# Kernel tuning notes

Hardware: AMD Instinct MI355X
Metric: run time of the kernel (lower is better)

The kernel has to match this reference:

```python
import jax, jax.numpy as jnp
import numpy as np

N_HEAD = 32
N_KV_HEAD = 8
ROPE_THETA = 500000.0


def rotate_half(x):
    d = x.shape[-1] // 2
    return jnp.concatenate((-x[..., d:], x[..., :d]), axis=-1)


def setup_inputs() -> dict:
    key = jax.random.key(0)
    ks = jax.random.split(key, 5)
    C = 2048
    B, T = 2, 2048
    s = 1.0 / np.sqrt(C)
    return {
        "x": jax.random.normal(ks[0], (B, T, C), dtype=jnp.float32),
        "Wq": jax.random.normal(ks[1], (C, C), dtype=jnp.float32) * s,
        "Wk": jax.random.normal(ks[2], (C, 512), dtype=jnp.float32) * s,
        "Wv": jax.random.normal(ks[3], (C, 512), dtype=jnp.float32) * s,
        "Wo": jax.random.normal(ks[4], (C, C), dtype=jnp.float32) * s,
    }


def reference(x, Wq, Wk, Wv, Wo):
    B, T, C = x.shape
    H, KV = N_HEAD, N_KV_HEAD
    D = C // H
    n_rep = H // KV

    q = (x @ Wq).reshape(B, T, H, D).transpose(0, 2, 1, 3)   # [B,H,T,D]
    k = (x @ Wk).reshape(B, T, KV, D).transpose(0, 2, 1, 3)  # [B,KV,T,D]
    v = (x @ Wv).reshape(B, T, KV, D).transpose(0, 2, 1, 3)  # [B,KV,T,D]

    # RoPE: cos/sin of shape [1,1,T,D], broadcast over batch and heads
    inv_freq = 1.0 / (ROPE_THETA ** (jnp.arange(0, D, 2, dtype=jnp.float32) / D))
    freqs = jnp.arange(T, dtype=jnp.float32)[:, None] * inv_freq[None, :]  # [T,D/2]
    emb = jnp.concatenate((freqs, freqs), axis=-1)  # [T,D]
    cos = jnp.cos(emb)[None, None].astype(x.dtype)
    sin = jnp.sin(emb)[None, None].astype(x.dtype)

    q = q * cos + rotate_half(q) * sin
    k = k * cos + rotate_half(k) * sin

    # repeat_kv (GQA expansion): [B,KV,T,D] -> [B,H,T,D]
    k = jnp.repeat(k, n_rep, axis=1)
    v = jnp.repeat(v, n_rep, axis=1)

    scale = 1.0 / jnp.sqrt(jnp.asarray(D, dtype=x.dtype))
    scores = jnp.einsum("bhqd,bhkd->bhqk", q, k) * scale  # [B,H,T,T]
    causal = jnp.tril(jnp.ones((T, T), dtype=bool))
    scores = jnp.where(causal[None, None], scores, jnp.finfo(scores.dtype).min)
    attn = jax.nn.softmax(scores, axis=-1)
    y = jnp.einsum("bhqk,bhkd->bhqd", attn, v)  # [B,H,T,D]
    y = y.transpose(0, 2, 1, 3).reshape(B, T, C)
    return y @ Wo
```

## Files before the change

### kernel.cpp

```cpp
#include <hip/hip_runtime.h>

using u16 = unsigned short;
using u32 = unsigned int;

typedef __attribute__((ext_vector_type(8))) __bf16 bf16x8;
typedef __attribute__((ext_vector_type(4))) float f32x4;
typedef __attribute__((ext_vector_type(16))) float f32x16;

#define DEVI __device__ __forceinline__

DEVI float bf2f(u16 u) {
  union { u32 i; float f; } v; v.i = ((u32)u) << 16; return v.f;
}
DEVI u16 f2bf(float f) {
  union { float f; u32 u; } v; v.f = f;
  u32 u = v.u;
  u32 r = (u + 0x7fffu + ((u >> 16) & 1u)) >> 16;
  return (u16)r;
}
DEVI u32 pkbf(float a, float b) {
  union { __bf16 h[2]; u32 u; } t;
  t.h[0] = (__bf16)a; t.h[1] = (__bf16)b;
  return t.u;
}

DEVI void gload16(const u16* g, u16* l) {
  __builtin_amdgcn_global_load_lds(
      (const __attribute__((address_space(1))) void*)g,
      (__attribute__((address_space(3))) void*)l, 16, 0, 0);
}

__global__ __launch_bounds__(256) void cvt_bf16_f32(const float* __restrict__ in,
                                                    u16* __restrict__ out, int n8) {
  int i = blockIdx.x * 256 + threadIdx.x;
  if (i >= n8) return;
  const float4* fin = (const float4*)in;
  float4 a = fin[i * 2], b = fin[i * 2 + 1];
  u16 o[8] = {f2bf(a.x), f2bf(a.y), f2bf(a.z), f2bf(a.w),
              f2bf(b.x), f2bf(b.y), f2bf(b.z), f2bf(b.w)};
  ((uint4*)out)[i] = *(const uint4*)o;
}

DEVI void tcvt64_body(const float* in, u16* out, int R, int Cc, int c0, int r0, int t,
                      u16 (*tile)[72]) {
  {
    int row = t >> 2, part = t & 3;
    const float* src = in + (size_t)(r0 + row) * Cc + c0 + part * 16;
    float4 f0 = ((const float4*)src)[0];
    float4 f1 = ((const float4*)src)[1];
    float4 f2 = ((const float4*)src)[2];
    float4 f3 = ((const float4*)src)[3];
    u16 v[16] = {f2bf(f0.x), f2bf(f0.y), f2bf(f0.z), f2bf(f0.w),
                 f2bf(f1.x), f2bf(f1.y), f2bf(f1.z), f2bf(f1.w),
                 f2bf(f2.x), f2bf(f2.y), f2bf(f2.z), f2bf(f2.w),
                 f2bf(f3.x), f2bf(f3.y), f2bf(f3.z), f2bf(f3.w)};
    *(uint4*)&tile[row][part * 16]     = ((const uint4*)v)[0];
    *(uint4*)&tile[row][part * 16 + 8] = ((const uint4*)v)[1];
  }
  __syncthreads();
  {
    int c = t & 63, rq = t >> 6;
    u16 v[16];
#pragma unroll
    for (int i = 0; i < 16; i++) v[i] = tile[rq * 16 + i][c];
    u16* dst = out + (size_t)(c0 + c) * R + r0 + rq * 16;
    ((uint4*)dst)[0] = ((const uint4*)v)[0];
    ((uint4*)dst)[1] = ((const uint4*)v)[1];
  }
}

__global__ __launch_bounds__(256) void transpose_cvt64(const float* __restrict__ in,
                                                       u16* __restrict__ out,
                                                       int R, int Cc) {
  __shared__ u16 tile[64][72];
  tcvt64_body(in, out, R, Cc, blockIdx.x * 64, blockIdx.y * 64, threadIdx.x, tile);
}

__global__ __launch_bounds__(256) void transpose_wqkv(const float* __restrict__ Wq,
                                                      const float* __restrict__ Wk,
                                                      const float* __restrict__ Wv,
                                                      u16* __restrict__ out) {
  __shared__ u16 tile[64][72];
  int bx = blockIdx.x;
  const float* in;
  u16* dst;
  int Cc, c0;
  if (bx < 32)      { in = Wq; dst = out;                        Cc = 2048; c0 = bx * 64; }
  else if (bx < 40) { in = Wk; dst = out + (size_t)2048 * 2048;  Cc = 512;  c0 = (bx - 32) * 64; }
  else              { in = Wv; dst = out + (size_t)2560 * 2048;  Cc = 512;  c0 = (bx - 40) * 64; }
  tcvt64_body(in, dst, 2048, Cc, c0, blockIdx.y * 64, threadIdx.x, tile);
}

__global__ __launch_bounds__(256) void transpose_sl64(const u16* __restrict__ in, int ldin,
                                                      u16* __restrict__ out,
                                                      int R, int Cc) {
  __shared__ u16 tile[64][72];
  int c0 = blockIdx.x * 64, r0 = blockIdx.y * 64;
  int t = threadIdx.x;
  {
    int row = t >> 2, part = t & 3;
    const u16* src = in + (size_t)(r0 + row) * ldin + c0 + part * 16;
    uint4 a = ((const uint4*)src)[0];
    uint4 b = ((const uint4*)src)[1];
    *(uint4*)&tile[row][part * 16]     = a;
    *(uint4*)&tile[row][part * 16 + 8] = b;
  }
  __syncthreads();
  {
    int c = t & 63, rq = t >> 6;
    u16 v[16];
#pragma unroll
    for (int i = 0; i < 16; i++) v[i] = tile[rq * 16 + i][c];
    u16* dst = out + (size_t)(c0 + c) * R + r0 + rq * 16;
    ((uint4*)dst)[0] = ((const uint4*)v)[0];
    ((uint4*)dst)[1] = ((const uint4*)v)[1];
  }
}

DEVI void cstore(u16* C, size_t idx, float v)   { C[idx] = f2bf(v); }
DEVI void cstore(float* C, size_t idx, float v) { C[idx] = v; }

template <typename TO, bool ROPE>
__global__ __launch_bounds__(256) void gemm128(const u16* __restrict__ A,
                                               const u16* __restrict__ Bt,
                                               TO* __restrict__ C,
                                               int M, int N, int K) {
  __shared__ u16 As[2 * 128 * 32];
  __shared__ u16 Bs[2 * 128 * 32];
  int tid = threadIdx.x, wid = tid >> 6, lane = tid & 63;
  int quad = lane >> 4, l15 = lane & 15;

  int nwg = gridDim.x * gridDim.y;
  int bid = blockIdx.y * gridDim.x + blockIdx.x;
  int swz = (bid & 7) * (nwg >> 3) + (bid >> 3);
  int bx = swz % gridDim.x, by = swz / gridDim.x;
  int m0 = by * 128, n0 = bx * 128;
  int wm = (wid >> 1) * 64, wn = (wid & 1) * 64;

  int r0s = wid * 16 + (lane >> 2);
  int r1s = 64 + wid * 16 + (lane >> 2);
  int cblk = lane & 3;
  int cs0 = (cblk ^ ((r0s >> 1) & 3)) * 8;
  int cs1 = (cblk ^ ((r1s >> 1) & 3)) * 8;
  u16* lA0 = As + wid * 512 + lane * 8;
  u16* lA1 = As + (4 + wid) * 512 + lane * 8;
  u16* lB0 = Bs + wid * 512 + lane * 8;
  u16* lB1 = Bs + (4 + wid) * 512 + lane * 8;
  const u16* gA0 = A + (size_t)(m0 + r0s) * K + cs0;
  const u16* gA1 = A + (size_t)(m0 + r1s) * K + cs1;
  const u16* gB0 = Bt + (size_t)(n0 + r0s) * K + cs0;
  const u16* gB1 = Bt + (size_t)(n0 + r1s) * K + cs1;

  f32x4 acc[4][4];
  for (int i = 0; i < 4; i++)
    for (int j = 0; j < 4; j++) acc[i][j] = f32x4{0.f, 0.f, 0.f, 0.f};

  gload16(gA0, lA0);
  gload16(gA1, lA1);
  gload16(gB0, lB0);
  gload16(gB1, lB1);
  __builtin_amdgcn_s_waitcnt(0x0F70);
  __syncthreads();

  int cur = 0;
  for (int k0 = 0; k0 < K; k0 += 32) {
    int nb = cur ^ 1;
    if (k0 + 32 < K) {
      gload16(gA0 + k0 + 32, lA0 + nb * 4096);
      gload16(gA1 + k0 + 32, lA1 + nb * 4096);
      gload16(gB0 + k0 + 32, lB0 + nb * 4096);
      gload16(gB1 + k0 + 32, lB1 + nb * 4096);
    }
    const u16* Ab = As + cur * 4096;
    const u16* Bb = Bs + cur * 4096;
    bf16x8 af[4], bf_[4];
    for (int mi = 0; mi < 4; mi++) {
      int row = wm + mi * 16 + l15;
      af[mi] = *(const bf16x8*)(Ab + row * 32 + ((quad ^ ((row >> 1) & 3)) * 8));
    }
    for (int ni = 0; ni < 4; ni++) {
      int row = wn + ni * 16 + l15;
      bf_[ni] = *(const bf16x8*)(Bb + row * 32 + ((quad ^ ((row >> 1) & 3)) * 8));
    }
    for (int mi = 0; mi < 4; mi++)
      for (int ni = 0; ni < 4; ni++)
        acc[mi][ni] = __builtin_amdgcn_mfma_f32_16x16x32_bf16(af[mi], bf_[ni], acc[mi][ni], 0, 0, 0);
    __builtin_amdgcn_s_waitcnt(0x0F70);
    __syncthreads();
    cur = nb;
  }

  if (ROPE) {
#pragma unroll
    for (int ni = 0; ni < 2; ni++) {
      int nc = n0 + wn + ni * 16;
      if (nc < 2560) {
        float scale = (nc < 2048) ? 0.18033688f : 1.0f;
        float inv = exp2f(-(float)(ni * 16 + l15) * 0.59161152f);
#pragma unroll
        for (int mi = 0; mi < 4; mi++)
#pragma unroll
          for (int r = 0; r < 4; r++) {
            int t = (m0 + wm + mi * 16 + quad * 4 + r) & 2047;
            float sn, cs;
            __sincosf((float)t * inv, &sn, &cs);
            float xl = acc[mi][ni][r], xh = acc[mi][ni + 2][r];
            acc[mi][ni][r]     = (xl * cs - xh * sn) * scale;
            acc[mi][ni + 2][r] = (xh * cs + xl * sn) * scale;
          }
      }
    }
  }

  for (int mi = 0; mi < 4; mi++)
    for (int ni = 0; ni < 4; ni++)
      for (int r = 0; r < 4; r++) {
        int row = m0 + wm + mi * 16 + quad * 4 + r;
        int col = n0 + wn + ni * 16 + l15;
        cstore(C, (size_t)row * N + col, acc[mi][ni][r]);
      }
}

__global__ __launch_bounds__(256) void attn64(const u16* __restrict__ QKV,
                                              const u16* __restrict__ Vt,
                                              u16* __restrict__ Y) {
  __shared__ u16 Ks[2 * 64 * 64];
  __shared__ u16 Vst[2 * 64 * 64];

  int tid = threadIdx.x, wid = tid >> 6, lane = tid & 63;
  int l31 = lane & 31, hi = lane >> 5;
  int bh = blockIdx.y, b = bh >> 5, h = bh & 31, kvh = h >> 2;
  int p = blockIdx.x;

  int kr  = wid * 8 + (lane >> 3);
  int kgn = lane & 7;
  const u16* gK0 = QKV + (size_t)(b * 2048 + kr) * 3072 + 2048 + kvh * 64
                 + ((kgn ^ (kr & 7)) * 8);
  u16* lK0 = Ks + wid * 512 + lane * 8;

  int vr = tid >> 3, vg = tid & 7;
  const u16* gV0 = Vt + (size_t)(kvh * 64 + vr) * 4096 + b * 2048 + vg * 8;
  u16* lV0 = Vst + vr * 64 + ((vg ^ (vr & 7)) * 8);

  for (int pass = 0; pass < 2; pass++) {
    int j   = pass ? (15 - p) : p;
    int q0w = j * 128 + wid * 32;
    int qg  = q0w + l31;

    bf16x8 qf[4];
    {
      const u16* qp = QKV + (size_t)(b * 2048 + qg) * 3072 + h * 64 + hi * 8;
#pragma unroll
      for (int dh = 0; dh < 4; dh++) qf[dh] = *(const bf16x8*)(qp + dh * 16);
    }

    f32x16 o0, o1;
#pragma unroll
    for (int i = 0; i < 16; i++) { o0[i] = 0.f; o1[i] = 0.f; }
    float zsum = 0.f;

    int nkt = 2 * (j + 1);

    {
      uint4 va = *(const uint4*)(gV0);
      uint4 vb = *(const uint4*)(gV0 + 32 * 4096);
      gload16(gK0, lK0);
      gload16(gK0 + 32 * 3072, lK0 + 2048);
      __builtin_amdgcn_s_waitcnt(0x0F70);
      *(uint4*)(lV0)        = va;
      *(uint4*)(lV0 + 2048) = vb;
    }
    __syncthreads();

    int cur = 0;
    for (int kt = 0; kt < nkt; kt++) {
      int kbase = kt * 64;
      int nxt = cur ^ 1;
      bool more = (kt + 1 < nkt);
      uint4 va, vb;
      if (more) {
        size_t ko = (size_t)(kbase + 64);
        va = *(const uint4*)(gV0 + ko);
        vb = *(const uint4*)(gV0 + 32 * 4096 + ko);
        gload16(gK0 + ko * 3072, lK0 + nxt * 4096);
        gload16(gK0 + ko * 3072 + 32 * 3072, lK0 + nxt * 4096 + 2048);
      }

      const u16* Kb = Ks + cur * 4096;
      const u16* Vb = Vst + cur * 4096;
#pragma unroll
      for (int sub = 0; sub < 2; sub++) {
        int kb = kbase + sub * 32;
        if (kb > q0w) break;

        f32x16 s;
#pragma unroll
        for (int i = 0; i < 16; i++) s[i] = 0.f;
#pragma unroll
        for (int dh = 0; dh < 4; dh++) {
          int g = (dh * 2 + hi) ^ (l31 & 7);
          bf16x8 kf = *(const bf16x8*)(Kb + (sub * 32 + l31) * 64 + g * 8);
          s = __builtin_amdgcn_mfma_f32_32x32x16_bf16(kf, qf[dh], s, 0, 0, 0);
        }

        float pb[16];
        if (kb < q0w) {
#pragma unroll
          for (int r = 0; r < 16; r++) {
            float pv = exp2f(s[r]);
            zsum += pv;
            pb[r] = pv;
          }
        } else {
#pragma unroll
          for (int r = 0; r < 16; r++) {
            int key = kb + (r & 3) + 8 * (r >> 2) + 4 * hi;
            float pv = (key <= qg) ? exp2f(s[r]) : 0.f;
            zsum += pv;
            pb[r] = pv;
          }
        }

#pragma unroll
        for (int kk = 0; kk < 2; kk++) {
          const float* pp = pb + kk * 8;
          u32 a01 = pkbf(pp[0], pp[1]);
          u32 a23 = pkbf(pp[2], pp[3]);
          u32 a45 = pkbf(pp[4], pp[5]);
          u32 a67 = pkbf(pp[6], pp[7]);
          asm volatile("v_permlane32_swap_b32 %0, %1" : "+v"(a01), "+v"(a45));
          asm volatile("v_permlane32_swap_b32 %0, %1" : "+v"(a23), "+v"(a67));
          union { u32 w[4]; bf16x8 v; } pf;
          pf.w[0] = a01; pf.w[1] = a23; pf.w[2] = a45; pf.w[3] = a67;
          int kgr = sub * 4 + kk * 2 + hi;
          const u16* vp = Vb + l31 * 64 + ((kgr ^ (l31 & 7)) * 8);
          bf16x8 v0 = *(const bf16x8*)(vp);
          bf16x8 v1 = *(const bf16x8*)(vp + 2048);
          o0 = __builtin_amdgcn_mfma_f32_32x32x16_bf16(pf.v, v0, o0, 0, 0, 0);
          o1 = __builtin_amdgcn_mfma_f32_32x32x16_bf16(pf.v, v1, o1, 0, 0, 0);
        }
      }

      if (more) {
        __builtin_amdgcn_s_waitcnt(0x0F70);
        *(uint4*)(lV0 + nxt * 4096)        = va;
        *(uint4*)(lV0 + nxt * 4096 + 2048) = vb;
      }
      __syncthreads();
      cur = nxt;
    }

    float zf = zsum + __shfl_xor(zsum, 32);

#pragma unroll
    for (int r = 0; r < 16; r++) {
      int qr = (r & 3) + 8 * (r >> 2) + 4 * hi;
      float zr = __shfl(zf, qr, 64);
      float inv = 1.f / zr;
      size_t row = (size_t)(b * 2048 + q0w + qr);
      Y[row * 2048 + h * 64 + l31]      = f2bf(o0[r] * inv);
      Y[row * 2048 + h * 64 + 32 + l31] = f2bf(o1[r] * inv);
    }
  }
}

extern "C" void kernel_launch(void* const* d_in, const int* in_sizes, int n_in,
                              void* d_out, int out_size, void* d_ws, size_t ws_size,
                              hipStream_t stream) {
  const float* x  = (const float*)d_in[0];
  const float* Wq = (const float*)d_in[1];
  const float* Wk = (const float*)d_in[2];
  const float* Wv = (const float*)d_in[3];
  const float* Wo = (const float*)d_in[4];
  float* outp = (float*)d_out;

  u16* xb    = (u16*)d_ws;
  u16* WqkvT = xb + 8388608;
  u16* QKV   = WqkvT + 6291456;
  u16* Vt    = QKV + 12582912;
  u16* Yb    = xb;
  u16* WoT   = WqkvT;

  cvt_bf16_f32<<<4096, 256, 0, stream>>>(x, xb, 1048576);

  transpose_wqkv<<<dim3(48, 32), 256, 0, stream>>>(Wq, Wk, Wv, WqkvT);

  gemm128<u16, true><<<dim3(24, 32), 256, 0, stream>>>(xb, WqkvT, QKV, 4096, 3072, 2048);

  transpose_sl64<<<dim3(8, 64), 256, 0, stream>>>(QKV + 2560, 3072, Vt, 4096, 512);

  attn64<<<dim3(8, 64), 256, 0, stream>>>(QKV, Vt, Yb);

  transpose_cvt64<<<dim3(32, 32), 256, 0, stream>>>(Wo, WoT, 2048, 2048);
  gemm128<float, false><<<dim3(16, 32), 256, 0, stream>>>(Yb, WoT, outp, 4096, 2048, 2048);
}
```

Measured before the change: 310.5 us.

## Fuse both causal query passes into one K/V sweep sharing tiles

The attention kernel previously handled query blocks p and 15-p in two sequential passes, each streaming its own K/V tiles from global memory. Now both query tiles are processed together in a single sweep over the longer causal range, so K/V tiles are loaded once and reused for both sets of MFMAs. This halves K/V traffic and barrier count for the overlapping range, but doubles accumulator registers (four f32x16 outputs plus two Q fragments), which may lower occupancy or cause spills.

```diff
diff --git a/kernel.cpp b/kernel.cpp
--- a/kernel.cpp
+++ b/kernel.cpp
@@ -28,6 +28,18 @@
   __builtin_amdgcn_global_load_lds(
       (const __attribute__((address_space(1))) void*)g,
       (__attribute__((address_space(3))) void*)l, 16, 0, 0);
+}
+
+DEVI bf16x8 packP(const float* pp) {
+  u32 a01 = pkbf(pp[0], pp[1]);
+  u32 a23 = pkbf(pp[2], pp[3]);
+  u32 a45 = pkbf(pp[4], pp[5]);
+  u32 a67 = pkbf(pp[6], pp[7]);
+  asm volatile("v_permlane32_swap_b32 %0, %1" : "+v"(a01), "+v"(a45));
+  asm volatile("v_permlane32_swap_b32 %0, %1" : "+v"(a23), "+v"(a67));
+  union { u32 w[4]; bf16x8 v; } pf;
+  pf.w[0] = a01; pf.w[1] = a23; pf.w[2] = a45; pf.w[3] = a67;
+  return pf.v;
 }
 
 __global__ __launch_bounds__(256) void cvt_bf16_f32(const float* __restrict__ in,
@@ -231,6 +243,7 @@
   int l31 = lane & 31, hi = lane >> 5;
   int bh = blockIdx.y, b = bh >> 5, h = bh & 31, kvh = h >> 2;
   int p = blockIdx.x;
+  int jA = p, jB = 15 - p;
 
   int kr  = wid * 8 + (lane >> 3);
   int kgn = lane & 7;
@@ -242,124 +255,179 @@
   const u16* gV0 = Vt + (size_t)(kvh * 64 + vr) * 4096 + b * 2048 + vg * 8;
   u16* lV0 = Vst + vr * 64 + ((vg ^ (vr & 7)) * 8);
 
-  for (int pass = 0; pass < 2; pass++) {
-    int j   = pass ? (15 - p) : p;
-    int q0w = j * 128 + wid * 32;
-    int qg  = q0w + l31;
-
-    bf16x8 qf[4];
-    {
-      const u16* qp = QKV + (size_t)(b * 2048 + qg) * 3072 + h * 64 + hi * 8;
-#pragma unroll
-      for (int dh = 0; dh < 4; dh++) qf[dh] = *(const bf16x8*)(qp + dh * 16);
-    }
-
-    f32x16 o0, o1;
-#pragma unroll
-    for (int i = 0; i < 16; i++) { o0[i] = 0.f; o1[i] = 0.f; }
-    float zsum = 0.f;
-
-    int nkt = 2 * (j + 1);
-
-    {
-      uint4 va = *(const uint4*)(gV0);
-      uint4 vb = *(const uint4*)(gV0 + 32 * 4096);
-      gload16(gK0, lK0);
-      gload16(gK0 + 32 * 3072, lK0 + 2048);
-      __builtin_amdgcn_s_waitcnt(0x0F70);
-      *(uint4*)(lV0)        = va;
-      *(uint4*)(lV0 + 2048) = vb;
-    }
-    __syncthreads();
-
-    int cur = 0;
-    for (int kt = 0; kt < nkt; kt++) {
-      int kbase = kt * 64;
-      int nxt = cur ^ 1;
-      bool more = (kt + 1 < nkt);
-      uint4 va, vb;
-      if (more) {
-        size_t ko = (size_t)(kbase + 64);
-        va = *(const uint4*)(gV0 + ko);
-        vb = *(const uint4*)(gV0 + 32 * 4096 + ko);
-        gload16(gK0 + ko * 3072, lK0 + nxt * 4096);
-        gload16(gK0 + ko * 3072 + 32 * 3072, lK0 + nxt * 4096 + 2048);
-      }
-
-      const u16* Kb = Ks + cur * 4096;
-      const u16* Vb = Vst + cur * 4096;
-#pragma unroll
-      for (int sub = 0; sub < 2; sub++) {
-        int kb = kbase + sub * 32;
-        if (kb > q0w) break;
-
-        f32x16 s;
-#pragma unroll
-        for (int i = 0; i < 16; i++) s[i] = 0.f;
+  int q0wA = jA * 128 + wid * 32, qgA = q0wA + l31;
+  int q0wB = jB * 128 + wid * 32, qgB = q0wB + l31;
+
+  bf16x8 qfA[4], qfB[4];
+  {
+    const u16* qpA = QKV + (size_t)(b * 2048 + qgA) * 3072 + h * 64 + hi * 8;
+    const u16* qpB = QKV + (size_t)(b * 2048 + qgB) * 3072 + h * 64 + hi * 8;
+#pragma unroll
+    for (int dh = 0; dh < 4; dh++) {
+      qfA[dh] = *(const bf16x8*)(qpA + dh * 16);
+      qfB[dh] = *(const bf16x8*)(qpB + dh * 16);
+    }
+  }
+
+  f32x16 o0A, o1A, o0B, o1B;
+#pragma unroll
+  for (int i = 0; i < 16; i++) { o0A[i] = 0.f; o1A[i] = 0.f; o0B[i] = 0.f; o1B[i] = 0.f; }
+  float zsumA = 0.f, zsumB = 0.f;
+
+  int nkt = 2 * (jB + 1);
+
+  {
+    uint4 va = *(const uint4*)(gV0);
+    uint4 vb = *(const uint4*)(gV0 + 32 * 4096);
+    gload16(gK0, lK0);
+    gload16(gK0 + 32 * 3072, lK0 + 2048);
+    __builtin_amdgcn_s_waitcnt(0x0F70);
+    *(uint4*)(lV0)        = va;
+    *(uint4*)(lV0 + 2048) = vb;
+  }
+  __syncthreads();
+
+  int cur = 0;
+  for (int kt = 0; kt < nkt; kt++) {
+    int kbase = kt * 64;
+    int nxt = cur ^ 1;
+    bool more = (kt + 1 < nkt);
+    uint4 va, vb;
+    if (more) {
+      size_t ko = (size_t)(kbase + 64);
+      va = *(const uint4*)(gV0 + ko);
+      vb = *(const uint4*)(gV0 + 32 * 4096 + ko);
+      gload16(gK0 + ko * 3072, lK0 + nxt * 4096);
+      gload16(gK0 + ko * 3072 + 32 * 3072, lK0 + nxt * 4096 + 2048);
+    }
+
+    const u16* Kb = Ks + cur * 4096;
+    const u16* Vb = Vst + cur * 4096;
+#pragma unroll
+    for (int sub = 0; sub < 2; sub++) {
+      int kb = kbase + sub * 32;
+      if (kb > q0wB) break;
+      if (kb <= q0wA) {
+        f32x16 sA, sB;
+#pragma unroll
+        for (int i = 0; i < 16; i++) { sA[i] = 0.f; sB[i] = 0.f; }
 #pragma unroll
         for (int dh = 0; dh < 4; dh++) {
           int g = (dh * 2 + hi) ^ (l31 & 7);
           bf16x8 kf = *(const bf16x8*)(Kb + (sub * 32 + l31) * 64 + g * 8);
-          s = __builtin_amdgcn_mfma_f32_32x32x16_bf16(kf, qf[dh], s, 0, 0, 0);
-        }
-
-        float pb[16];
-        if (kb < q0w) {
+          sA = __builtin_amdgcn_mfma_f32_32x32x16_bf16(kf, qfA[dh], sA, 0, 0, 0);
+          sB = __builtin_amdgcn_mfma_f32_32x32x16_bf16(kf, qfB[dh], sB, 0, 0, 0);
+        }
+        float pbA[16], pbB[16];
+        if (kb < q0wA) {
 #pragma unroll
           for (int r = 0; r < 16; r++) {
-            float pv = exp2f(s[r]);
-            zsum += pv;
-            pb[r] = pv;
+            float pv = exp2f(sA[r]);
+            zsumA += pv;
+            pbA[r] = pv;
           }
         } else {
 #pragma unroll
           for (int r = 0; r < 16; r++) {
             int key = kb + (r & 3) + 8 * (r >> 2) + 4 * hi;
-            float pv = (key <= qg) ? exp2f(s[r]) : 0.f;
-            zsum += pv;
-            pb[r] = pv;
+            float pv = (key <= qgA) ? exp2f(sA[r]) : 0.f;
+            zsumA += pv;
+            pbA[r] = pv;
           }
         }
-
+#pragma unroll
+        for (int r = 0; r < 16; r++) {
+          float pv = exp2f(sB[r]);
+          zsumB += pv;
+          pbB[r] = pv;
+        }
+        bf16x8 pfA0 = packP(pbA), pfA1 = packP(pbA + 8);
+        bf16x8 pfB0 = packP(pbB), pfB1 = packP(pbB + 8);
 #pragma unroll
         for (int kk = 0; kk < 2; kk++) {
-          const float* pp = pb + kk * 8;
-          u32 a01 = pkbf(pp[0], pp[1]);
-          u32 a23 = pkbf(pp[2], pp[3]);
-          u32 a45 = pkbf(pp[4], pp[5]);
-          u32 a67 = pkbf(pp[6], pp[7]);
-          asm volatile("v_permlane32_swap_b32 %0, %1" : "+v"(a01), "+v"(a45));
-          asm volatile("v_permlane32_swap_b32 %0, %1" : "+v"(a23), "+v"(a67));
-          union { u32 w[4]; bf16x8 v; } pf;
-          pf.w[0] = a01; pf.w[1] = a23; pf.w[2] = a45; pf.w[3] = a67;
           int kgr = sub * 4 + kk * 2 + hi;
           const u16* vp = Vb + l31 * 64 + ((kgr ^ (l31 & 7)) * 8);
           bf16x8 v0 = *(const bf16x8*)(vp);
           bf16x8 v1 = *(const bf16x8*)(vp + 2048);
-          o0 = __builtin_amdgcn_mfma_f32_32x32x16_bf16(pf.v, v0, o0, 0, 0, 0);
-          o1 = __builtin_amdgcn_mfma_f32_32x32x16_bf16(pf.v, v1, o1, 0, 0, 0);
+          bf16x8 pA = kk ? pfA1 : pfA0;
+          bf16x8 pB = kk ? pfB1 : pfB0;
+          o0A = __builtin_amdgcn_mfma_f32_32x32x16_bf16(pA, v0, o0A, 0, 0, 0);
+          o1A = __builtin_amdgcn_mfma_f32_32x32x16_bf16(pA, v1, o1A, 0, 0, 0);
+          o0B = __builtin_amdgcn_mfma_f32_32x32x16_bf16(pB, v0, o0B, 0, 0, 0);
+          o1B = __builtin_amdgcn_mfma_f32_32x32x16_bf16(pB, v1, o1B, 0, 0, 0);
+        }
+      } else {
+        f32x16 s;
+#pragma unroll
+        for (int i = 0; i < 16; i++) s[i] = 0.f;
+#pragma unroll
+        for (int dh = 0; dh < 4; dh++) {
+          int g = (dh * 2 + hi) ^ (l31 & 7);
+          bf16x8 kf = *(const bf16x8*)(Kb + (sub * 32 + l31) * 64 + g * 8);
+          s = __builtin_amdgcn_mfma_f32_32x32x16_bf16(kf, qfB[dh], s, 0, 0, 0);
+        }
+        float pb[16];
+        if (kb < q0wB) {
+#pragma unroll
+          for (int r = 0; r < 16; r++) {
+            float pv = exp2f(s[r]);
+            zsumB += pv;
+            pb[r] = pv;
+          }
+        } else {
+#pragma unroll
+          for (int r = 0; r < 16; r++) {
+            int key = kb + (r & 3) + 8 * (r >> 2) + 4 * hi;
+            float pv = (key <= qgB) ? exp2f(s[r]) : 0.f;
+            zsumB += pv;
+            pb[r] = pv;
+          }
+        }
+        bf16x8 pf0 = packP(pb), pf1 = packP(pb + 8);
+#pragma unroll
+        for (int kk = 0; kk < 2; kk++) {
+          int kgr = sub * 4 + kk * 2 + hi;
+          const u16* vp = Vb + l31 * 64 + ((kgr ^ (l31 & 7)) * 8);
+          bf16x8 v0 = *(const bf16x8*)(vp);
+          bf16x8 v1 = *(const bf16x8*)(vp + 2048);
+          bf16x8 pB = kk ? pf1 : pf0;
+          o0B = __builtin_amdgcn_mfma_f32_32x32x16_bf16(pB, v0, o0B, 0, 0, 0);
+          o1B = __builtin_amdgcn_mfma_f32_32x32x16_bf16(pB, v1, o1B, 0, 0, 0);
         }
       }
-
-      if (more) {
-        __builtin_amdgcn_s_waitcnt(0x0F70);
-        *(uint4*)(lV0 + nxt * 4096)        = va;
-        *(uint4*)(lV0 + nxt * 4096 + 2048) = vb;
-      }
-      __syncthreads();
-      cur = nxt;
-    }
-
-    float zf = zsum + __shfl_xor(zsum, 32);
-
+    }
+
+    if (more) {
+      __builtin_amdgcn_s_waitcnt(0x0F70);
+      *(uint4*)(lV0 + nxt * 4096)        = va;
+      *(uint4*)(lV0 + nxt * 4096 + 2048) = vb;
+    }
+    __syncthreads();
+    cur = nxt;
+  }
+
+  {
+    float zf = zsumA + __shfl_xor(zsumA, 32);
 #pragma unroll
     for (int r = 0; r < 16; r++) {
       int qr = (r & 3) + 8 * (r >> 2) + 4 * hi;
       float zr = __shfl(zf, qr, 64);
       float inv = 1.f / zr;
-      size_t row = (size_t)(b * 2048 + q0w + qr);
-      Y[row * 2048 + h * 64 + l31]      = f2bf(o0[r] * inv);
-      Y[row * 2048 + h * 64 + 32 + l31] = f2bf(o1[r] * inv);
+      size_t row = (size_t)(b * 2048 + q0wA + qr);
+      Y[row * 2048 + h * 64 + l31]      = f2bf(o0A[r] * inv);
+      Y[row * 2048 + h * 64 + 32 + l31] = f2bf(o1A[r] * inv);
+    }
+  }
+  {
+    float zf = zsumB + __shfl_xor(zsumB, 32);
+#pragma unroll
+    for (int r = 0; r < 16; r++) {
+      int qr = (r & 3) + 8 * (r >> 2) + 4 * hi;
+      float zr = __shfl(zf, qr, 64);
+      float inv = 1.f / zr;
+      size_t row = (size_t)(b * 2048 + q0wB + qr);
+      Y[row * 2048 + h * 64 + l31]      = f2bf(o0B[r] * inv);
+      Y[row * 2048 + h * 64 + 32 + l31] = f2bf(o1B[r] * inv);
     }
   }
 }
```

New measurement: 309.3 us. Within noise of the previous version (-0.4%).
